# Kernel tuning notes

Hardware: AMD Instinct MI355X
Metric: run time of the kernel (lower is better)

The kernel has to match this reference:

```python
import jax, jax.numpy as jnp
import numpy as np
from jax import lax

HIDDEN = 16
DN = ('NCHW', 'OIHW', 'NCHW')

def setup_inputs() -> dict:
    key = jax.random.key(0)
    k1, k2, k3 = jax.random.split(key, 3)
    b, t, c, h, w = 8, 12, 5, 256, 256
    x = jax.random.normal(k1, (b, t, c, h, w), dtype=jnp.float32)
    # PyTorch-like init scale for conv weights
    W_cell = jax.random.normal(k2, (4 * HIDDEN, c + HIDDEN, 3, 3), dtype=jnp.float32) * 0.05
    b_cell = jnp.zeros((4 * HIDDEN,), dtype=jnp.float32)
    W_final = jax.random.normal(k3, (1, HIDDEN, 1, 1), dtype=jnp.float32) * 0.1
    b_final = jnp.zeros((1,), dtype=jnp.float32)
    return {"x": x, "W_cell": W_cell, "b_cell": b_cell,
            "W_final": W_final, "b_final": b_final}

def _cell_step(h_c, x_t, W_cell, b_cell):
    h_cur, c_cur = h_c
    combined = jnp.concatenate([x_t, h_cur], axis=1)          # [B, C+H, H, W]
    conv = lax.conv_general_dilated(combined, W_cell, (1, 1), 'SAME',
                                    dimension_numbers=DN)
    conv = conv + b_cell[None, :, None, None]                  # [B, 4H, H, W]
    cc_i, cc_f, cc_o, cc_g = jnp.split(conv, 4, axis=1)
    i = jax.nn.sigmoid(cc_i)
    f = jax.nn.sigmoid(cc_f)
    o = jax.nn.sigmoid(cc_o)
    g = jnp.tanh(cc_g)
    c_next = f * c_cur + i * g
    h_next = o * jnp.tanh(c_next)
    return h_next, c_next

def reference(x, W_cell, b_cell, W_final, b_final):
    b, t, c, hh, ww = x.shape
    h0 = jnp.zeros((b, HIDDEN, hh, ww), dtype=x.dtype)
    c0 = jnp.zeros((b, HIDDEN, hh, ww), dtype=x.dtype)
    xt = jnp.moveaxis(x, 1, 0)  # [T, B, C, H, W] for scan over time

    def step(carry, x_t):
        return _cell_step(carry, x_t, W_cell, b_cell), None

    (h_last, _), _ = lax.scan(step, (h0, c0), xt)
    out = lax.conv_general_dilated(h_last, W_final, (1, 1), 'SAME',
                                   dimension_numbers=DN)
    out = out + b_final[None, :, None, None]
    return out
```

## Files before the change

kernel.cpp:

```cpp
#include <hip/hip_runtime.h>
#include <hip/hip_cooperative_groups.h>
#include <math.h>

#define HIDDEN 16
#define CIN 5
#define BB 8
#define TT 12
#define HH 256
#define WW 256
#define TX 32
#define TY 8
#define HALO_X 34
#define HALO_Y 10
#define NPX (HALO_X * HALO_Y)
#define STRIDE 40
#define NBLK_PERSIST 1024

typedef __attribute__((ext_vector_type(8))) short bf16x8;
typedef __attribute__((ext_vector_type(4))) float floatx4;

namespace cg = cooperative_groups;

__device__ __forceinline__ unsigned short f2bf(float f) {
    unsigned int u = __float_as_uint(f);
    u += 0x7fffu + ((u >> 16) & 1u);
    return (unsigned short)(u >> 16);
}
__device__ __forceinline__ float bf2f(unsigned short s) {
    return __uint_as_float(((unsigned int)s) << 16);
}
__device__ __forceinline__ float fast_sigmoid(float x) { return 1.0f / (1.0f + __expf(-x)); }
__device__ __forceinline__ float fast_tanh(float x) {
    float e2 = __expf(-2.0f * fabsf(x));
    float t = (1.0f - e2) / (1.0f + e2);
    return copysignf(t, x);
}

__global__ void prep_w_kernel(const float* __restrict__ Wc,
                              unsigned short* __restrict__ Wfrag) {
    int i = blockIdx.x * 256 + threadIdx.x;
    if (i >= 9 * 4 * 64 * 8) return;
    int j    = i & 7;
    int lane = (i >> 3) & 63;
    int g    = (i >> 9) & 3;
    int tap  = i >> 11;
    int k    = ((lane >> 4) << 3) + j;
    int col  = lane & 15;
    int o    = g * 16 + col;
    float w  = 0.0f;
    if (k < 21) {
        int ci_ref = (k < 16) ? (5 + k) : (k - 16);
        w = Wc[(o * 21 + ci_ref) * 9 + tap];
    }
    Wfrag[i] = f2bf(w);
}

__global__ void prep_x_kernel(const float* __restrict__ x,
                              unsigned short* __restrict__ xp) {
    size_t n = (size_t)blockIdx.x * 256 + threadIdx.x;
    const size_t TOTPX = (size_t)BB * TT * HH * WW;
    if (n >= TOTPX) return;
    size_t bt  = n / (size_t)(HH * WW);
    size_t pix = n - bt * (size_t)(HH * WW);
    const float* src = x + bt * (size_t)CIN * HH * WW + pix;
    unsigned short v[8];
    #pragma unroll
    for (int c = 0; c < CIN; ++c) v[c] = f2bf(src[(size_t)c * HH * WW]);
    v[5] = 0; v[6] = 0; v[7] = 0;
    *(uint4*)&xp[n * 8] = *(const uint4*)v;
}

__global__ __launch_bounds__(256, 4)
void convlstm_persistent_kernel(const float* __restrict__ x,
                                const unsigned short* __restrict__ xp,
                                unsigned short* __restrict__ ha,
                                unsigned short* __restrict__ hbuf,
                                const unsigned short* __restrict__ Wfrag,
                                const float* __restrict__ bias,
                                const float* __restrict__ Wf,
                                const float* __restrict__ bfin,
                                float* __restrict__ out,
                                int use_xp) {
    __shared__ unsigned short tile[NPX * STRIDE];
    cg::grid_group grid = cg::this_grid();

    const int tid  = threadIdx.x;
    const int lane = tid & 63;
    const int wave = tid >> 6;
    const int u    = lane & 15;
    const int quad = lane >> 4;

    float bg[4];
    #pragma unroll
    for (int g = 0; g < 4; ++g) bg[g] = bias[g * 16 + u];
    const float wfu = Wf[u];
    const float bf0 = bfin[0];

    float cA[2][2][4];
    float cB[2][2][4];
    #pragma unroll
    for (int a = 0; a < 2; ++a)
        #pragma unroll
        for (int m = 0; m < 2; ++m)
            #pragma unroll
            for (int r = 0; r < 4; ++r) { cA[a][m][r] = 0.0f; cB[a][m][r] = 0.0f; }

    #pragma unroll 1
    for (int t = 0; t < TT; ++t) {
        const unsigned short* h_in  = (t & 1) ? ha : hbuf;
        unsigned short*       h_out = (t & 1) ? hbuf : ha;
        const int first = (t == 0);
        const int last  = (t == TT - 1);

        #pragma unroll
        for (int tl = 0; tl < 2; ++tl) {
            const int n  = (int)blockIdx.x + tl * NBLK_PERSIST;
            const int x0 = (n & 7) * TX;
            const int y0 = ((n >> 3) & 31) * TY;
            const int bb = n >> 8;

            if (t > 0 || tl > 0) __syncthreads();

            for (int i = tid; i < NPX; i += 256) {
                int ly = i / HALO_X;
                int lx = i - ly * HALO_X;
                int gy = y0 + ly - 1;
                int gx = x0 + lx - 1;
                bool inb = (gy >= 0 && gy < HH && gx >= 0 && gx < WW);
                unsigned short* row = &tile[i * STRIDE];
                uint4 z = {0, 0, 0, 0};
                if (inb && !first) {
                    size_t hbase = ((size_t)bb * HH * WW + (size_t)gy * WW + gx) * HIDDEN;
                    *(uint4*)&row[0] = *(const uint4*)&h_in[hbase];
                    *(uint4*)&row[8] = *(const uint4*)&h_in[hbase + 8];
                } else {
                    *(uint4*)&row[0] = z;
                    *(uint4*)&row[8] = z;
                }
                if (use_xp) {
                    if (inb) {
                        size_t xb = (((size_t)bb * TT + t) * (size_t)(HH * WW)
                                     + (size_t)gy * WW + gx) * 8;
                        *(uint4*)&row[16] = *(const uint4*)&xp[xb];
                    } else {
                        *(uint4*)&row[16] = z;
                    }
                } else {
                    #pragma unroll
                    for (int ci = 0; ci < CIN; ++ci) {
                        float v = 0.0f;
                        if (inb) v = x[(((size_t)bb * TT + t) * CIN + ci) * (size_t)(HH * WW)
                                       + (size_t)gy * WW + gx];
                        row[16 + ci] = f2bf(v);
                    }
                    row[21] = 0; row[22] = 0; row[23] = 0;
                }
                *(uint4*)&row[24] = z;
            }
            __syncthreads();

            #pragma unroll 1
            for (int half = 0; half < 2; ++half) {
                floatx4 acc[2][4];
                int abase[2];
                #pragma unroll
                for (int mh = 0; mh < 2; ++mh) {
                    int ml = half * 2 + mh;
                    int m  = wave + ml * 4;
                    int my = m >> 1;
                    int mx = (m & 1) << 4;
                    abase[mh] = (my * HALO_X + mx + u) * STRIDE + quad * 8;
                    #pragma unroll
                    for (int g = 0; g < 4; ++g)
                        acc[mh][g] = (floatx4){bg[g], bg[g], bg[g], bg[g]};
                }

                #pragma unroll 3
                for (int tap = 0; tap < 9; ++tap) {
                    int ky = tap / 3;
                    int kx = tap - ky * 3;
                    int toff = (ky * HALO_X + kx) * STRIDE;
                    bf16x8 bfr[4];
                    #pragma unroll
                    for (int g = 0; g < 4; ++g)
                        bfr[g] = *(const bf16x8*)&Wfrag[(size_t)((tap * 4 + g) * 64 + lane) * 8];
                    #pragma unroll
                    for (int mh = 0; mh < 2; ++mh) {
                        bf16x8 af = *(const bf16x8*)&tile[abase[mh] + toff];
                        #pragma unroll
                        for (int g = 0; g < 4; ++g)
                            acc[mh][g] = __builtin_amdgcn_mfma_f32_16x16x32_bf16(
                                af, bfr[g], acc[mh][g], 0, 0, 0);
                    }
                }

                #pragma unroll
                for (int mh = 0; mh < 2; ++mh) {
                    int ml = half * 2 + mh;
                    int m  = wave + ml * 4;
                    int my = m >> 1;
                    int mx = (m & 1) << 4;
                    int py = y0 + my;
                    #pragma unroll
                    for (int r = 0; r < 4; ++r) {
                        int pxx = x0 + mx + quad * 4 + r;
                        float ig = fast_sigmoid(acc[mh][0][r]);
                        float fg = fast_sigmoid(acc[mh][1][r]);
                        float og = fast_sigmoid(acc[mh][2][r]);
                        float gg = fast_tanh(acc[mh][3][r]);
                        float c_old = half ? cB[tl][mh][r] : cA[tl][mh][r];
                        float c_new = fg * c_old + ig * gg;
                        if (half) cB[tl][mh][r] = c_new; else cA[tl][mh][r] = c_new;
                        float hval = og * fast_tanh(c_new);
                        if (last) {
                            float s = wfu * hval;
                            s += __shfl_xor(s, 1);
                            s += __shfl_xor(s, 2);
                            s += __shfl_xor(s, 4);
                            s += __shfl_xor(s, 8);
                            if (u == 0)
                                out[(size_t)bb * HH * WW + (size_t)py * WW + pxx] = s + bf0;
                        } else {
                            size_t idx = ((size_t)bb * HH * WW + (size_t)py * WW + pxx)
                                         * HIDDEN + u;
                            h_out[idx] = f2bf(hval);
                        }
                    }
                }
            }
        }
        if (t != TT - 1) grid.sync();
    }
}

__global__ __launch_bounds__(256, 5)
void convlstm_step_kernel(const float* __restrict__ x, int t,
                          const unsigned short* __restrict__ xp,
                          const unsigned short* __restrict__ h_in,
                          unsigned short* __restrict__ h_out,
                          float* __restrict__ c_state,
                          const unsigned short* __restrict__ Wfrag,
                          const float* __restrict__ bias,
                          int first, int use_xp) {
    __shared__ unsigned short tile[NPX * STRIDE];

    const int tid  = threadIdx.x;
    const int lane = tid & 63;
    const int wave = tid >> 6;
    const int x0 = blockIdx.x * TX;
    const int y0 = blockIdx.y * TY;
    const int bb = blockIdx.z;

    for (int i = tid; i < NPX; i += 256) {
        int ly = i / HALO_X;
        int lx = i - ly * HALO_X;
        int gy = y0 + ly - 1;
        int gx = x0 + lx - 1;
        bool inb = (gy >= 0 && gy < HH && gx >= 0 && gx < WW);
        unsigned short* row = &tile[i * STRIDE];
        uint4 z = {0, 0, 0, 0};
        if (inb && !first) {
            size_t hbase = ((size_t)bb * HH * WW + (size_t)gy * WW + gx) * HIDDEN;
            *(uint4*)&row[0] = *(const uint4*)&h_in[hbase];
            *(uint4*)&row[8] = *(const uint4*)&h_in[hbase + 8];
        } else {
            *(uint4*)&row[0] = z;
            *(uint4*)&row[8] = z;
        }
        if (use_xp) {
            if (inb) {
                size_t xb = (((size_t)bb * TT + t) * (size_t)(HH * WW)
                             + (size_t)gy * WW + gx) * 8;
                *(uint4*)&row[16] = *(const uint4*)&xp[xb];
            } else {
                *(uint4*)&row[16] = z;
            }
        } else {
            #pragma unroll
            for (int ci = 0; ci < CIN; ++ci) {
                float v = 0.0f;
                if (inb) v = x[(((size_t)bb * TT + t) * CIN + ci) * (size_t)(HH * WW)
                               + (size_t)gy * WW + gx];
                row[16 + ci] = f2bf(v);
            }
            row[21] = 0; row[22] = 0; row[23] = 0;
        }
        *(uint4*)&row[24] = z;
    }
    __syncthreads();

    const int u    = lane & 15;
    const int quad = lane >> 4;

    float bg[4];
    #pragma unroll
    for (int g = 0; g < 4; ++g) bg[g] = bias[g * 16 + u];

    #pragma unroll 1
    for (int half = 0; half < 2; ++half) {
        floatx4 acc[2][4];
        int abase[2];
        #pragma unroll
        for (int mh = 0; mh < 2; ++mh) {
            int ml = half * 2 + mh;
            int m  = wave + ml * 4;
            int my = m >> 1;
            int mx = (m & 1) << 4;
            abase[mh] = (my * HALO_X + mx + u) * STRIDE + quad * 8;
            #pragma unroll
            for (int g = 0; g < 4; ++g)
                acc[mh][g] = (floatx4){bg[g], bg[g], bg[g], bg[g]};
        }

        #pragma unroll 3
        for (int tap = 0; tap < 9; ++tap) {
            int ky = tap / 3;
            int kx = tap - ky * 3;
            int toff = (ky * HALO_X + kx) * STRIDE;
            bf16x8 bfr[4];
            #pragma unroll
            for (int g = 0; g < 4; ++g)
                bfr[g] = *(const bf16x8*)&Wfrag[(size_t)((tap * 4 + g) * 64 + lane) * 8];
            #pragma unroll
            for (int mh = 0; mh < 2; ++mh) {
                bf16x8 af = *(const bf16x8*)&tile[abase[mh] + toff];
                #pragma unroll
                for (int g = 0; g < 4; ++g)
                    acc[mh][g] = __builtin_amdgcn_mfma_f32_16x16x32_bf16(
                        af, bfr[g], acc[mh][g], 0, 0, 0);
            }
        }

        #pragma unroll
        for (int mh = 0; mh < 2; ++mh) {
            int ml = half * 2 + mh;
            int m  = wave + ml * 4;
            int my = m >> 1;
            int mx = (m & 1) << 4;
            int py = y0 + my;
            #pragma unroll
            for (int r = 0; r < 4; ++r) {
                int pxx = x0 + mx + quad * 4 + r;
                size_t idx = ((size_t)bb * HH * WW + (size_t)py * WW + pxx) * HIDDEN + u;
                float ig = fast_sigmoid(acc[mh][0][r]);
                float fg = fast_sigmoid(acc[mh][1][r]);
                float og = fast_sigmoid(acc[mh][2][r]);
                float gg = fast_tanh(acc[mh][3][r]);
                float c_old = first ? 0.0f : c_state[idx];
                float c_new = fg * c_old + ig * gg;
                c_state[idx] = c_new;
                h_out[idx] = f2bf(og * fast_tanh(c_new));
            }
        }
    }
}

__global__ void final_conv_kernel(const unsigned short* __restrict__ h,
                                  const float* __restrict__ Wf,
                                  const float* __restrict__ bf_,
                                  float* __restrict__ out) {
    int i = blockIdx.x * 256 + threadIdx.x;
    if (i >= BB * HH * WW) return;
    size_t base = (size_t)i * HIDDEN;
    uint4 v0 = *(const uint4*)&h[base];
    uint4 v1 = *(const uint4*)&h[base + 8];
    const unsigned short* p0 = (const unsigned short*)&v0;
    const unsigned short* p1 = (const unsigned short*)&v1;
    float s = bf_[0];
    #pragma unroll
    for (int k = 0; k < 8; ++k) s += Wf[k] * bf2f(p0[k]);
    #pragma unroll
    for (int k = 0; k < 8; ++k) s += Wf[8 + k] * bf2f(p1[k]);
    out[i] = s;
}

extern "C" void kernel_launch(void* const* d_in, const int* in_sizes, int n_in,
                              void* d_out, int out_size, void* d_ws, size_t ws_size,
                              hipStream_t stream) {
    const float* x  = (const float*)d_in[0];
    const float* Wc = (const float*)d_in[1];
    const float* bc = (const float*)d_in[2];
    const float* Wf = (const float*)d_in[3];
    const float* bf = (const float*)d_in[4];
    float* out = (float*)d_out;

    char* ws = (char*)d_ws;
    const size_t h_bytes = (size_t)BB * HH * WW * HIDDEN * 2;
    const size_t c_bytes = (size_t)BB * HH * WW * HIDDEN * 4;
    const size_t w_bytes = 9 * 4 * 64 * 8 * 2;
    const size_t x_bytes = (size_t)BB * TT * HH * WW * 8 * 2;

    unsigned short* h_a = (unsigned short*)(ws);
    unsigned short* h_b = (unsigned short*)(ws + h_bytes);
    float* c            = (float*)(ws + 2 * h_bytes);
    unsigned short* Wfr = (unsigned short*)(ws + 2 * h_bytes + c_bytes);
    unsigned short* xp  = (unsigned short*)(ws + 2 * h_bytes + c_bytes + w_bytes);

    const int use_xp =
        (ws_size >= 2 * h_bytes + c_bytes + w_bytes + x_bytes) ? 1 : 0;

    prep_w_kernel<<<(9 * 4 * 64 * 8 + 255) / 256, 256, 0, stream>>>(Wc, Wfr);
    if (use_xp) {
        size_t totpx = (size_t)BB * TT * HH * WW;
        prep_x_kernel<<<(int)((totpx + 255) / 256), 256, 0, stream>>>(x, xp);
    }

    int occ = 0;
    hipOccupancyMaxActiveBlocksPerMultiprocessor(&occ, convlstm_persistent_kernel,
                                                 256, 0);
    bool done = false;
    if (occ >= 4) {
        const unsigned short* xp_arg = use_xp ? xp : (const unsigned short*)0;
        int use_xp_arg = use_xp;
        void* kargs[] = {
            (void*)&x, (void*)&xp_arg, (void*)&h_a, (void*)&h_b,
            (void*)&Wfr, (void*)&bc, (void*)&Wf, (void*)&bf,
            (void*)&out, (void*)&use_xp_arg
        };
        if (hipLaunchCooperativeKernel((const void*)convlstm_persistent_kernel,
                                       dim3(NBLK_PERSIST, 1, 1), dim3(256, 1, 1),
                                       kargs, 0, stream) == hipSuccess)
            done = true;
    }

    if (!done) {
        dim3 grid(WW / TX, HH / TY, BB);
        dim3 block(256, 1, 1);
        const unsigned short* h_in = h_a;
        for (int t = 0; t < TT; ++t) {
            unsigned short* h_out = (t & 1) ? h_b : h_a;
            convlstm_step_kernel<<<grid, block, 0, stream>>>(
                x, t, use_xp ? xp : (const unsigned short*)0,
                h_in, h_out, c, Wfr, bc, (t == 0) ? 1 : 0, use_xp);
            h_in = h_out;
        }
        final_conv_kernel<<<(BB * HH * WW + 255) / 256, 256, 0, stream>>>(
            h_in, Wf, bf, out);
    }
}
```

Before: 686.2 us.

## Replace grid-wide barrier with per-tile neighbor flag synchronization

Removes the cooperative-groups grid.sync between time steps. Instead, each tile publishes a per-tile step counter in global memory, and before each step one wave spins until its 3x3 neighbor tiles have finished the previous step. Halo-load offsets are also precomputed once per block, which cuts repeated index arithmetic and 64-bit math. The point is to let blocks run ahead without a global barrier. In exchange it adds spin-polling, fence traffic and an extra flag-reset kernel, and it depends on every block being co-resident.

Result: slower. 700.4 us (+2.1%).

```diff
diff --git a/kernel.cpp b/kernel.cpp
--- a/kernel.cpp
+++ b/kernel.cpp
@@ -1,5 +1,4 @@
 #include <hip/hip_runtime.h>
-#include <hip/hip_cooperative_groups.h>
 #include <math.h>
 
 #define HIDDEN 16
@@ -15,11 +14,10 @@
 #define NPX (HALO_X * HALO_Y)
 #define STRIDE 40
 #define NBLK_PERSIST 1024
+#define NTILES 2048
 
 typedef __attribute__((ext_vector_type(8))) short bf16x8;
 typedef __attribute__((ext_vector_type(4))) float floatx4;
-
-namespace cg = cooperative_groups;
 
 __device__ __forceinline__ unsigned short f2bf(float f) {
     unsigned int u = __float_as_uint(f);
@@ -70,6 +68,11 @@
     *(uint4*)&xp[n * 8] = *(const uint4*)v;
 }
 
+__global__ void prep_flags_kernel(unsigned int* __restrict__ flags) {
+    int i = blockIdx.x * 256 + threadIdx.x;
+    if (i < NTILES) flags[i] = 0;
+}
+
 __global__ __launch_bounds__(256, 4)
 void convlstm_persistent_kernel(const float* __restrict__ x,
                                 const unsigned short* __restrict__ xp,
@@ -80,15 +83,62 @@
                                 const float* __restrict__ Wf,
                                 const float* __restrict__ bfin,
                                 float* __restrict__ out,
+                                unsigned int* __restrict__ flags,
                                 int use_xp) {
     __shared__ unsigned short tile[NPX * STRIDE];
-    cg::grid_group grid = cg::this_grid();
 
     const int tid  = threadIdx.x;
     const int lane = tid & 63;
     const int wave = tid >> 6;
     const int u    = lane & 15;
     const int quad = lane >> 4;
+    const int bid  = (int)blockIdx.x;
+
+    int nb_id[2];
+    unsigned nb_act = 0;
+    {
+        int s  = lane + (lane >= 4 ? 1 : 0);
+        int dy = s / 3 - 1;
+        int dx = s - (s / 3) * 3 - 1;
+        #pragma unroll
+        for (int tl = 0; tl < 2; ++tl) {
+            int n  = bid + tl * NBLK_PERSIST;
+            int tx = n & 7;
+            int ty = (n >> 3) & 31;
+            bool act = (lane < 8) && (tx + dx >= 0) && (tx + dx < 8)
+                                  && (ty + dy >= 0) && (ty + dy < 32);
+            nb_id[tl] = act ? (n + dy * 8 + dx) : 0;
+            if (act) nb_act |= 1u << tl;
+        }
+    }
+
+    int hof[2][2];
+    int xof[2][2];
+    int pixv[2][2];
+    int bbv[2];
+    unsigned inbm = 0;
+    #pragma unroll
+    for (int tl = 0; tl < 2; ++tl) {
+        int n  = bid + tl * NBLK_PERSIST;
+        int x0 = (n & 7) * TX;
+        int y0 = ((n >> 3) & 31) * TY;
+        int bb = n >> 8;
+        bbv[tl] = bb;
+        #pragma unroll
+        for (int it = 0; it < 2; ++it) {
+            int i  = tid + it * 256;
+            int ly = i / HALO_X;
+            int lx = i - ly * HALO_X;
+            int gy = y0 + ly - 1;
+            int gx = x0 + lx - 1;
+            bool inb = (gy >= 0 && gy < HH && gx >= 0 && gx < WW) && (i < NPX);
+            int pix = gy * WW + gx;
+            pixv[tl][it] = pix;
+            hof[tl][it]  = (bb * HH * WW + pix) * HIDDEN;
+            xof[tl][it]  = (bb * TT * HH * WW + pix) * 8;
+            if (inb) inbm |= 1u << (tl * 2 + it);
+        }
+    }
 
     float bg[4];
     #pragma unroll
@@ -114,43 +164,56 @@
 
         #pragma unroll
         for (int tl = 0; tl < 2; ++tl) {
-            const int n  = (int)blockIdx.x + tl * NBLK_PERSIST;
+            const int n  = bid + tl * NBLK_PERSIST;
             const int x0 = (n & 7) * TX;
             const int y0 = ((n >> 3) & 31) * TY;
-            const int bb = n >> 8;
-
-            if (t > 0 || tl > 0) __syncthreads();
-
-            for (int i = tid; i < NPX; i += 256) {
-                int ly = i / HALO_X;
-                int lx = i - ly * HALO_X;
-                int gy = y0 + ly - 1;
-                int gx = x0 + lx - 1;
-                bool inb = (gy >= 0 && gy < HH && gx >= 0 && gx < WW);
-                unsigned short* row = &tile[i * STRIDE];
+            const int bb = bbv[tl];
+
+            if (t > 0) {
+                if (wave == 0) {
+                    const bool act = (nb_act >> tl) & 1;
+                    const unsigned need = (unsigned)t;
+                    for (;;) {
+                        unsigned v = act
+                            ? __hip_atomic_load(&flags[nb_id[tl]], __ATOMIC_RELAXED,
+                                                __HIP_MEMORY_SCOPE_AGENT)
+                            : 0xFFFFFFFFu;
+                        if (__all(v >= need)) break;
+                        __builtin_amdgcn_s_sleep(2);
+                    }
+                    if (tid == 0) __threadfence();
+                }
+                __syncthreads();
+            } else if (tl == 1) {
+                __syncthreads();
+            }
+
+            #pragma unroll
+            for (int it = 0; it < 2; ++it) {
+                if (it == 1 && tid >= NPX - 256) break;
+                unsigned short* row = &tile[(tid + it * 256) * STRIDE];
+                const bool inb = (inbm >> (tl * 2 + it)) & 1;
                 uint4 z = {0, 0, 0, 0};
                 if (inb && !first) {
-                    size_t hbase = ((size_t)bb * HH * WW + (size_t)gy * WW + gx) * HIDDEN;
-                    *(uint4*)&row[0] = *(const uint4*)&h_in[hbase];
-                    *(uint4*)&row[8] = *(const uint4*)&h_in[hbase + 8];
+                    const unsigned short* hp = h_in + hof[tl][it];
+                    *(uint4*)&row[0] = *(const uint4*)&hp[0];
+                    *(uint4*)&row[8] = *(const uint4*)&hp[8];
                 } else {
                     *(uint4*)&row[0] = z;
                     *(uint4*)&row[8] = z;
                 }
                 if (use_xp) {
-                    if (inb) {
-                        size_t xb = (((size_t)bb * TT + t) * (size_t)(HH * WW)
-                                     + (size_t)gy * WW + gx) * 8;
-                        *(uint4*)&row[16] = *(const uint4*)&xp[xb];
-                    } else {
+                    if (inb)
+                        *(uint4*)&row[16] =
+                            *(const uint4*)&xp[xof[tl][it] + t * (HH * WW * 8)];
+                    else
                         *(uint4*)&row[16] = z;
-                    }
                 } else {
                     #pragma unroll
                     for (int ci = 0; ci < CIN; ++ci) {
                         float v = 0.0f;
                         if (inb) v = x[(((size_t)bb * TT + t) * CIN + ci) * (size_t)(HH * WW)
-                                       + (size_t)gy * WW + gx];
+                                       + pixv[tl][it]];
                         row[16 + ci] = f2bf(v);
                     }
                     row[21] = 0; row[22] = 0; row[23] = 0;
@@ -228,8 +291,16 @@
                     }
                 }
             }
-        }
-        if (t != TT - 1) grid.sync();
+
+            if (!last) {
+                __syncthreads();
+                if (tid == 0) {
+                    __threadfence();
+                    __hip_atomic_store(&flags[n], (unsigned)(t + 1), __ATOMIC_RELAXED,
+                                       __HIP_MEMORY_SCOPE_AGENT);
+                }
+            }
+        }
     }
 }
 
@@ -388,18 +459,21 @@
     const size_t h_bytes = (size_t)BB * HH * WW * HIDDEN * 2;
     const size_t c_bytes = (size_t)BB * HH * WW * HIDDEN * 4;
     const size_t w_bytes = 9 * 4 * 64 * 8 * 2;
+    const size_t f_bytes = (size_t)NTILES * 4;
     const size_t x_bytes = (size_t)BB * TT * HH * WW * 8 * 2;
 
     unsigned short* h_a = (unsigned short*)(ws);
     unsigned short* h_b = (unsigned short*)(ws + h_bytes);
     float* c            = (float*)(ws + 2 * h_bytes);
     unsigned short* Wfr = (unsigned short*)(ws + 2 * h_bytes + c_bytes);
-    unsigned short* xp  = (unsigned short*)(ws + 2 * h_bytes + c_bytes + w_bytes);
+    unsigned int* flags = (unsigned int*)(ws + 2 * h_bytes + c_bytes + w_bytes);
+    unsigned short* xp  = (unsigned short*)(ws + 2 * h_bytes + c_bytes + w_bytes + f_bytes);
 
     const int use_xp =
-        (ws_size >= 2 * h_bytes + c_bytes + w_bytes + x_bytes) ? 1 : 0;
+        (ws_size >= 2 * h_bytes + c_bytes + w_bytes + f_bytes + x_bytes) ? 1 : 0;
 
     prep_w_kernel<<<(9 * 4 * 64 * 8 + 255) / 256, 256, 0, stream>>>(Wc, Wfr);
+    prep_flags_kernel<<<(NTILES + 255) / 256, 256, 0, stream>>>(flags);
     if (use_xp) {
         size_t totpx = (size_t)BB * TT * HH * WW;
         prep_x_kernel<<<(int)((totpx + 255) / 256), 256, 0, stream>>>(x, xp);
@@ -415,7 +489,7 @@
         void* kargs[] = {
             (void*)&x, (void*)&xp_arg, (void*)&h_a, (void*)&h_b,
             (void*)&Wfr, (void*)&bc, (void*)&Wf, (void*)&bf,
-            (void*)&out, (void*)&use_xp_arg
+            (void*)&out, (void*)&flags, (void*)&use_xp_arg
         };
         if (hipLaunchCooperativeKernel((const void*)convlstm_persistent_kernel,
                                        dim3(NBLK_PERSIST, 1, 1), dim3(256, 1, 1),
```
